# Optimization experiments

Hardware: AMD Instinct MI355X
Metric: run time of the kernel (lower is better)

The kernel has to match this reference:

```python
import jax, jax.numpy as jnp
import numpy as np

B = 4096      # batch
D = 64        # state_dim
H = 512       # hidden_dim


def setup_inputs() -> dict:
    key = jax.random.key(0)
    ks = jax.random.split(key, 16)

    def init(k, shape, fan_in):
        return jax.random.normal(k, shape, dtype=jnp.float32) / np.float32(np.sqrt(fan_in))

    mu = jax.random.normal(ks[0], (B, D), dtype=jnp.float32)
    sigma_diag = 0.1 * jax.random.uniform(ks[1], (B, D), dtype=jnp.float32) + 0.01
    states = jnp.concatenate([mu, sigma_diag], axis=1)  # [B, 2D]

    return {
        "t": jnp.float32(0.5),
        "states": states,
        # dynamics net: tanh MLP D -> H -> H -> D
        "W1": init(ks[2], (H, D), D), "b1": jnp.zeros((H,), jnp.float32),
        "W2": init(ks[3], (H, H), H), "b2": jnp.zeros((H,), jnp.float32),
        "W3": init(ks[4], (D, H), H), "b3": jnp.zeros((D,), jnp.float32),
        # process-noise net: tanh MLP D -> H -> H -> D, softplus head (diagonal Q)
        "V1": init(ks[5], (H, D), D), "c1": jnp.zeros((H,), jnp.float32),
        "V2": init(ks[6], (H, H), H), "c2": jnp.zeros((H,), jnp.float32),
        "V3": init(ks[7], (D, H), H), "c3": jnp.zeros((D,), jnp.float32),
    }


def reference(t, states, W1, b1, W2, b2, W3, b3, V1, c1, V2, c2, V3, c3):
    # UPN ODE function, diagonal-covariance path.
    mu = states[:, :D]          # [B, D]
    sigma_diag = states[:, D:]  # [B, D]

    # dynamics MLP forward (t is an autonomous-system placeholder, unused)
    h1 = jnp.tanh(mu @ W1.T + b1)   # [B, H]
    h2 = jnp.tanh(h1 @ W2.T + b2)   # [B, H]
    mu_drift = h2 @ W3.T + b3       # [B, D]

    # analytic batched Jacobian of the tanh MLP: J = W3 diag(1-h2^2) W2 diag(1-h1^2) W1
    d1 = 1.0 - h1 * h1              # [B, H]
    d2 = 1.0 - h2 * h2              # [B, H]
    inner = jnp.einsum('hk,bk,kd->bhd', W2, d1, W1)   # [B, H, D]
    J = jnp.einsum('oh,bh,bhd->bod', W3, d2, inner)   # [B, D, D]
    J_diag = jnp.diagonal(J, axis1=1, axis2=2)        # [B, D]

    # process-noise net: diagonal Q, softplus ensures positivity
    g1 = jnp.tanh(mu @ V1.T + c1)
    g2 = jnp.tanh(g1 @ V2.T + c2)
    Q_diag = jax.nn.softplus(g2 @ V3.T + c3)          # [B, D]

    sigma_drift = 2.0 * J_diag * sigma_diag + Q_diag  # [B, D]
    return jnp.concatenate([mu_drift, sigma_drift], axis=1)  # [B, 2D]
```

## Files before the change

### kernel.cpp

```cpp
#include <hip/hip_runtime.h>
#include <hip/hip_bf16.h>

#define BB 4096
#define DD 64
#define HH 512

typedef __hip_bfloat16 bf16;
typedef _Float16 f16;
typedef __attribute__((ext_vector_type(8))) short bf16x8;
typedef __attribute__((ext_vector_type(8))) _Float16 f16x8;
typedef __attribute__((ext_vector_type(4))) float f32x4;

__device__ __forceinline__ float bf2f(bf16 x) { return __bfloat162float(x); }
__device__ __forceinline__ float u16tof(unsigned short u) {
  union { unsigned int i; float f; } v; v.i = ((unsigned int)u) << 16; return v.f;
}
#define BC8(p) __builtin_bit_cast(bf16x8, *(const uint4*)(p))
#define BCH8(p) __builtin_bit_cast(f16x8, *(const uint4*)(p))

__device__ __forceinline__ void gl16(const void* g, void* l) {
  __builtin_amdgcn_global_load_lds((__attribute__((address_space(1))) void*)g,
                                   (__attribute__((address_space(3))) void*)l,
                                   16, 0, 0);
}


__global__ __launch_bounds__(256) void cvt_weights(
    const float* __restrict__ W2, const float* __restrict__ V2,
    const float* __restrict__ W1, const float* __restrict__ V1,
    const float* __restrict__ W3, const float* __restrict__ V3,
    bf16* __restrict__ W2bf, bf16* __restrict__ V2bf,
    bf16* __restrict__ W1bf, bf16* __restrict__ V1bf,
    bf16* __restrict__ W3bf, bf16* __restrict__ V3bf,
    f16* __restrict__ W2fr, f16* __restrict__ W1sw, float* __restrict__ W3T) {
  int blk = blockIdx.x, t = threadIdx.x;
  if (blk < 512) {
    const float* src = (blk < 256) ? W2 : V2;
    bf16* dst = (blk < 256) ? W2bf : V2bf;
    int i = ((blk & 255) * 256 + t) * 4;
    float4 v = *(const float4*)(src + i);
    bf16 o[4] = {__float2bfloat16(v.x), __float2bfloat16(v.y),
                 __float2bfloat16(v.z), __float2bfloat16(v.w)};
    *(uint2*)(dst + i) = *(uint2*)o;
  } else if (blk < 640) {
    int uid = (blk - 512) * 256 + t;
    int col = (uid >> 2) & 511;
    int kc2s = uid >> 11;
    int kc = kc2s >> 1, s = kc2s & 1, q = uid & 3;
    const float* src = W2 + (size_t)col * HH + kc * 64 + s * 32 + q * 8;
    float4 a = *(const float4*)src;
    float4 b = *(const float4*)(src + 4);
    f16 o[8] = {(f16)a.x, (f16)a.y, (f16)a.z, (f16)a.w,
                (f16)b.x, (f16)b.y, (f16)b.z, (f16)b.w};
    *(uint4*)(W2fr + (size_t)uid * 8) = *(uint4*)o;
  } else if (blk < 656) {
    int uid = (blk - 640) * 256 + t;
    int kc = uid >> 9, rem = uid & 511;
    int dl = rem >> 3, u = rem & 7;
    f16 o[8];
#pragma unroll
    for (int e = 0; e < 8; ++e)
      o[e] = (f16)W1[(size_t)(kc * 64 + u * 8 + e) * DD + dl];
    *(uint4*)(W1sw + (size_t)((kc * 64 + dl) * 8 + (u ^ (dl & 7))) * 8) = *(uint4*)o;
  } else if (blk < 784) {
    int which = (blk - 656) >> 5;
    int local = (blk - 656) & 31;
    const float* src = (which == 0) ? W1 : (which == 1) ? V1 : (which == 2) ? W3 : V3;
    bf16* dst = (which == 0) ? W1bf : (which == 1) ? V1bf : (which == 2) ? W3bf : V3bf;
    int i = (local * 256 + t) * 4;
    float4 v = *(const float4*)(src + i);
    bf16 o[4] = {__float2bfloat16(v.x), __float2bfloat16(v.y),
                 __float2bfloat16(v.z), __float2bfloat16(v.w)};
    *(uint2*)(dst + i) = *(uint2*)o;
  } else {
    int e = ((blk - 784) * 256 + t) * 4;
    int h = e >> 6, o0 = e & 63;
    float o[4];
#pragma unroll
    for (int j = 0; j < 4; ++j) o[j] = W3[(size_t)(o0 + j) * HH + h];
    *(float4*)(W3T + (size_t)h * 64 + o0) = *(float4*)o;
  }
}

__global__ __launch_bounds__(256) void fwd(
    const float* __restrict__ states,
    const bf16* __restrict__ W1bf, const float* __restrict__ b1,
    const bf16* __restrict__ W2bf, const float* __restrict__ b2,
    const bf16* __restrict__ W3bf, const float* __restrict__ b3,
    const bf16* __restrict__ V1bf, const float* __restrict__ c1,
    const bf16* __restrict__ V2bf, const float* __restrict__ c2,
    const bf16* __restrict__ V3bf, const float* __restrict__ c3,
    bf16* __restrict__ Xbf, bf16* __restrict__ Ybf, float* __restrict__ out) {
  __shared__ __align__(16) bf16 mus[16 * 72];
  __shared__ __align__(16) bf16 Xres[16 * 520];
  __shared__ __align__(16) bf16 Bs[128 * 72];
  __shared__ __align__(16) bf16 Ych[16 * 136];
  const int bt = blockIdx.x * 16;
  const int path = blockIdx.y;
  const bf16* Wa = path ? V1bf : W1bf;
  const float* ba = path ? c1 : b1;
  const bf16* Wb = path ? V2bf : W2bf;
  const float* bbv = path ? c2 : b2;
  const bf16* Wc = path ? V3bf : W3bf;
  const float* bcv = path ? c3 : b3;
  const int t = threadIdx.x;
  const int lane = t & 63;
  const int w = t >> 6;
  const int c = lane & 15, q = lane >> 4;

  if (t < 128) {
    int row = t >> 3, cg = (t & 7) * 8;
    bf16 o[8];
#pragma unroll
    for (int j = 0; j < 8; j += 4) {
      float4 v = *(const float4*)(states + (size_t)(bt + row) * 128 + cg + j);
      o[j] = __float2bfloat16(v.x); o[j + 1] = __float2bfloat16(v.y);
      o[j + 2] = __float2bfloat16(v.z); o[j + 3] = __float2bfloat16(v.w);
    }
    *(uint4*)(mus + row * 72 + cg) = *(const uint4*)o;
  }
  __syncthreads();

  for (int nch = 0; nch < 4; ++nch) {
    if (nch) __syncthreads();
#pragma unroll
    for (int i = 0; i < 4; ++i) {
      int g = t + i * 256;
      int row = g >> 3, kb = (g & 7) * 8;
      *(uint4*)(Bs + row * 72 + kb) =
          *(const uint4*)(Wa + (size_t)(nch * 128 + row) * 64 + kb);
    }
    __syncthreads();
    f32x4 acc1[2] = {};
#pragma unroll
    for (int s = 0; s < 2; ++s) {
      bf16x8 af = BC8(mus + c * 72 + s * 32 + q * 8);
#pragma unroll
      for (int nt = 0; nt < 2; ++nt) {
        bf16x8 bfr = BC8(Bs + (w * 32 + nt * 16 + c) * 72 + s * 32 + q * 8);
        acc1[nt] = __builtin_amdgcn_mfma_f32_16x16x32_bf16(af, bfr, acc1[nt], 0, 0, 0);
      }
    }
#pragma unroll
    for (int nt = 0; nt < 2; ++nt) {
      int col = nch * 128 + w * 32 + nt * 16 + c;
      float bias = ba[col];
#pragma unroll
      for (int r = 0; r < 4; ++r) {
        int row = q * 4 + r;
        float x = tanhf(acc1[nt][r] + bias);
        Xres[row * 520 + col] = __float2bfloat16(x);
        if (!path) Xbf[(size_t)(bt + row) * HH + col] = __float2bfloat16(x);
      }
    }
  }
  __syncthreads();

  f32x4 acc3 = {};
  for (int hch = 0; hch < 4; ++hch) {
    f32x4 acc2[2] = {};
    for (int kc = 0; kc < 8; ++kc) {
      __syncthreads();
#pragma unroll
      for (int i = 0; i < 4; ++i) {
        int g = t + i * 256;
        int row = g >> 3, kb = (g & 7) * 8;
        *(uint4*)(Bs + row * 72 + kb) =
            *(const uint4*)(Wb + (size_t)(hch * 128 + row) * HH + kc * 64 + kb);
      }
      __syncthreads();
#pragma unroll
      for (int s = 0; s < 2; ++s) {
        bf16x8 af = BC8(Xres + c * 520 + kc * 64 + s * 32 + q * 8);
#pragma unroll
        for (int nt = 0; nt < 2; ++nt) {
          bf16x8 bfr = BC8(Bs + (w * 32 + nt * 16 + c) * 72 + s * 32 + q * 8);
          acc2[nt] = __builtin_amdgcn_mfma_f32_16x16x32_bf16(af, bfr, acc2[nt], 0, 0, 0);
        }
      }
    }
    __syncthreads();
#pragma unroll
    for (int nt = 0; nt < 2; ++nt) {
      int hl = w * 32 + nt * 16 + c;
      int h = hch * 128 + hl;
      float bias = bbv[h];
#pragma unroll
      for (int r = 0; r < 4; ++r) {
        int row = q * 4 + r;
        float y = tanhf(acc2[nt][r] + bias);
        Ych[row * 136 + hl] = __float2bfloat16(y);
        if (!path) Ybf[(size_t)(bt + row) * HH + h] = __float2bfloat16(y);
      }
    }
    __syncthreads();
#pragma unroll
    for (int s3 = 0; s3 < 4; ++s3) {
      bf16x8 bf3 = BC8(Wc + (size_t)(w * 16 + c) * HH + hch * 128 + s3 * 32 + q * 8);
      bf16x8 af3 = BC8(Ych + c * 136 + s3 * 32 + q * 8);
      acc3 = __builtin_amdgcn_mfma_f32_16x16x32_bf16(af3, bf3, acc3, 0, 0, 0);
    }
  }
  {
    int o = w * 16 + c;
    float bias = bcv[o];
#pragma unroll
    for (int r = 0; r < 4; ++r) {
      int row = q * 4 + r;
      float v = acc3[r] + bias;
      if (path) {
        v = fmaxf(v, 0.0f) + log1pf(expf(-fabsf(v)));
        out[(size_t)(bt + row) * 128 + 64 + o] = v;
      } else {
        out[(size_t)(bt + row) * 128 + o] = v;
      }
    }
  }
}

#define LDSW1 0
#define LDSD1 65536
#define LDSD2 73728
#define LDSRED 77824

__global__ __launch_bounds__(512, 2) void k4_gemm(
    const bf16* __restrict__ Xbf, const bf16* __restrict__ Ybf,
    const f16* __restrict__ W1sw, const f16* __restrict__ W2fr,
    const float* __restrict__ W3T, float* __restrict__ Jpart) {
  __shared__ __align__(16) char lds[81920];
  const int bt = blockIdx.x;
  const int h0 = blockIdx.y * 256;
  const int t = threadIdx.x;
  const int lane = t & 63;
  const int w = t >> 6;
  const int c = lane & 15, q = lane >> 4;
  const int wr = w >> 2, wc = w & 3;
  const int b0 = bt * 4;

#pragma unroll
  for (int i = 0; i < 8; ++i)
    gl16((const char*)W1sw + (t + i * 512) * 16,
         (char*)lds + LDSW1 + (t + i * 512) * 16);
  {
    int e = t * 4, j = e >> 9, k = e & 511;
    ushort4 xv = *(const ushort4*)((const unsigned short*)Xbf +
                                   (size_t)(b0 + j) * HH + k);
    f16 o[4];
    float x;
    x = u16tof(xv.x); o[0] = (f16)(1.f - x * x);
    x = u16tof(xv.y); o[1] = (f16)(1.f - x * x);
    x = u16tof(xv.z); o[2] = (f16)(1.f - x * x);
    x = u16tof(xv.w); o[3] = (f16)(1.f - x * x);
    *(uint2*)(lds + LDSD1 + e * 2) = *(uint2*)o;
  }
  {
    int e = t * 2, j = e >> 8, n = e & 255;
    ushort2 yv = *(const ushort2*)((const unsigned short*)Ybf +
                                   (size_t)(b0 + j) * HH + h0 + n);
    float y0 = u16tof(yv.x), y1 = u16tof(yv.y);
    float2 d2v = {1.f - y0 * y0, 1.f - y1 * y1};
    *(float2*)(lds + LDSD2 + e * 4) = d2v;
  }
  __syncthreads();

  const int cj = c & 7;
  const int j16_0 = ((0 + q) ^ cj) * 16;
  const int j16_1 = ((4 + q) ^ cj) * 16;
  const int arow = c * 128;
  const char* d1b = (const char*)lds + LDSD1 + wr * 2048 + q * 16;

  const char* gB = (const char*)W2fr + (size_t)(h0 + wc * 64) * 64 +
                   (c * 64 + q * 16);
#define BLD(kc_, s_, nt_) \
  BCH8(gB + ((kc_) * 2 + (s_)) * 32768 + (nt_) * 1024)

  f16x8 bb0[2][4], bb1[2][4];
#pragma unroll
  for (int nt = 0; nt < 4; ++nt) bb0[0][nt] = BLD(0, 0, nt);
#pragma unroll
  for (int nt = 0; nt < 4; ++nt) bb1[0][nt] = BLD(0, 1, nt);

  f32x4 acc[8][4] = {};

#pragma unroll
  for (int kc = 0; kc < 8; ++kc) {
    const int cur = kc & 1, nxt = cur ^ 1;
    if (kc < 7) {
#pragma unroll
      for (int nt = 0; nt < 4; ++nt) bb0[nxt][nt] = BLD(kc + 1, 0, nt);
#pragma unroll
      for (int nt = 0; nt < 4; ++nt) bb1[nxt][nt] = BLD(kc + 1, 1, nt);
    }
    const char* Ab = (const char*)lds + LDSW1 + kc * 8192;
    f16x8 a0[4], a1[4];
#pragma unroll
    for (int i = 0; i < 4; ++i) a0[i] = BCH8(Ab + arow + i * 2048 + j16_0);
#pragma unroll
    for (int i = 0; i < 4; ++i) a1[i] = BCH8(Ab + arow + i * 2048 + j16_1);
    f16x8 d00 = BCH8(d1b + kc * 128);
    f16x8 d10 = BCH8(d1b + 1024 + kc * 128);
    f16x8 d01 = BCH8(d1b + 64 + kc * 128);
    f16x8 d11 = BCH8(d1b + 1024 + 64 + kc * 128);

    f16x8 av;
    __builtin_amdgcn_s_setprio(1);
#pragma unroll
    for (int mt = 0; mt < 4; ++mt) {
      av = a0[mt] * d00;
#pragma unroll
      for (int nt = 0; nt < 4; ++nt)
        acc[mt][nt] = __builtin_amdgcn_mfma_f32_16x16x32_f16(
            av, bb0[cur][nt], acc[mt][nt], 0, 0, 0);
    }
#pragma unroll
    for (int mt = 0; mt < 4; ++mt) {
      av = a0[mt] * d10;
#pragma unroll
      for (int nt = 0; nt < 4; ++nt)
        acc[mt + 4][nt] = __builtin_amdgcn_mfma_f32_16x16x32_f16(
            av, bb0[cur][nt], acc[mt + 4][nt], 0, 0, 0);
    }
#pragma unroll
    for (int mt = 0; mt < 4; ++mt) {
      av = a1[mt] * d01;
#pragma unroll
      for (int nt = 0; nt < 4; ++nt)
        acc[mt][nt] = __builtin_amdgcn_mfma_f32_16x16x32_f16(
            av, bb1[cur][nt], acc[mt][nt], 0, 0, 0);
    }
#pragma unroll
    for (int mt = 0; mt < 4; ++mt) {
      av = a1[mt] * d11;
#pragma unroll
      for (int nt = 0; nt < 4; ++nt)
        acc[mt + 4][nt] = __builtin_amdgcn_mfma_f32_16x16x32_f16(
            av, bb1[cur][nt], acc[mt + 4][nt], 0, 0, 0);
    }
    __builtin_amdgcn_s_setprio(0);
    __builtin_amdgcn_sched_barrier(0);
  }
  __syncthreads();

#pragma unroll
  for (int i = 0; i < 8; ++i) {
    int e = (t + i * 512) * 4;
    int col = e >> 6, dl0 = e & 63;
    float4 v = *(const float4*)(W3T + (size_t)(h0 + col) * 64 + dl0);
    *(float4*)(lds + (col * 72 + dl0) * 4) = v;
  }
  __syncthreads();

  float d2r[2][4];
#pragma unroll
  for (int bh = 0; bh < 2; ++bh)
#pragma unroll
    for (int nt = 0; nt < 4; ++nt)
      d2r[bh][nt] = *(const float*)(
          lds + LDSD2 + ((wr * 2 + bh) * 256 + wc * 64 + nt * 16 + c) * 4);

  float vsum[8][4] = {};
#pragma unroll
  for (int mt4 = 0; mt4 < 4; ++mt4)
#pragma unroll
    for (int nt = 0; nt < 4; ++nt) {
      f32x4 w3v = *(const f32x4*)(
          lds + ((wc * 64 + nt * 16 + c) * 72 + mt4 * 16 + q * 4) * 4);
#pragma unroll
      for (int bh = 0; bh < 2; ++bh) {
        const int mt = bh * 4 + mt4;
        float sc = d2r[bh][nt];
#pragma unroll
        for (int r = 0; r < 4; ++r)
          vsum[mt][r] += acc[mt][nt][r] * w3v[r] * sc;
      }
    }

#pragma unroll
  for (int mt = 0; mt < 8; ++mt)
#pragma unroll
    for (int r = 0; r < 4; ++r) {
      float v = vsum[mt][r];
      v += __shfl_xor(v, 1);
      v += __shfl_xor(v, 2);
      v += __shfl_xor(v, 4);
      v += __shfl_xor(v, 8);
      if (c == 0)
        *(float*)(lds + LDSRED +
                  (wc * 256 + wr * 128 + mt * 16 + q * 4 + r) * 4) = v;
    }
  __syncthreads();
  if (t < 256) {
    float J = *(const float*)(lds + LDSRED + t * 4) +
              *(const float*)(lds + LDSRED + (256 + t) * 4) +
              *(const float*)(lds + LDSRED + (512 + t) * 4) +
              *(const float*)(lds + LDSRED + (768 + t) * 4);
    Jpart[(size_t)blockIdx.y * (BB * 64) + (size_t)bt * 256 + t] = J;
  }
}

__global__ __launch_bounds__(256) void combine(
    const float* __restrict__ Jpart, const float* __restrict__ states,
    float* __restrict__ out) {
  int idx = blockIdx.x * 256 + threadIdx.x;
  int b = idx >> 6, d = idx & 63;
  const int plane = BB * 64;
  float J = Jpart[idx] + Jpart[plane + idx];
  float sig = states[(size_t)b * 128 + 64 + d];
  float qd = out[(size_t)b * 128 + 64 + d];
  out[(size_t)b * 128 + 64 + d] = 2.0f * J * sig + qd;
}

extern "C" void kernel_launch(void* const* d_in, const int* in_sizes, int n_in,
                              void* d_out, int out_size, void* d_ws, size_t ws_size,
                              hipStream_t stream) {
  const float* states = (const float*)d_in[1];
  const float* W1 = (const float*)d_in[2];
  const float* b1 = (const float*)d_in[3];
  const float* W2 = (const float*)d_in[4];
  const float* b2 = (const float*)d_in[5];
  const float* W3 = (const float*)d_in[6];
  const float* b3 = (const float*)d_in[7];
  const float* V1 = (const float*)d_in[8];
  const float* c1 = (const float*)d_in[9];
  const float* V2 = (const float*)d_in[10];
  const float* c2 = (const float*)d_in[11];
  const float* V3 = (const float*)d_in[12];
  const float* c3 = (const float*)d_in[13];
  float* out = (float*)d_out;

  bf16* Xbf = (bf16*)d_ws;
  bf16* Ybf = Xbf + (size_t)BB * HH;
  bf16* W2bf = Ybf + (size_t)BB * HH;
  bf16* V2bf = W2bf + (size_t)HH * HH;
  bf16* W1bf = V2bf + (size_t)HH * HH;
  bf16* V1bf = W1bf + (size_t)HH * DD;
  bf16* W3bf = V1bf + (size_t)HH * DD;
  bf16* V3bf = W3bf + (size_t)DD * HH;
  f16* W1sw = (f16*)(V3bf + (size_t)DD * HH);
  f16* W2fr = W1sw + (size_t)DD * HH;
  float* W3T = (float*)(W2fr + (size_t)HH * HH);
  float* Jpart = W3T + (size_t)HH * DD;

  cvt_weights<<<dim3(816), 256, 0, stream>>>(W2, V2, W1, V1, W3, V3,
                                             W2bf, V2bf, W1bf, V1bf,
                                             W3bf, V3bf, W2fr, W1sw, W3T);
  fwd<<<dim3(256, 2), 256, 0, stream>>>(states, W1bf, b1, W2bf, b2, W3bf, b3,
                                        V1bf, c1, V2bf, c2, V3bf, c3,
                                        Xbf, Ybf, out);
  k4_gemm<<<dim3(1024, 2), 512, 0, stream>>>(Xbf, Ybf, W1sw, W2fr, W3T, Jpart);
  combine<<<dim3(1024), 256, 0, stream>>>(Jpart, states, out);
}
```

Before: 269.2 us.

## Split Jacobian GEMM per batch row and K-half for more blocks

The Jacobian-diagonal kernel now gives each block a single batch row and half of the hidden K range, with 256 threads instead of 512. That makes a 4096x2x2 grid of smaller-LDS blocks meant to raise occupancy, and the combine kernel now sums four partial planes. W3 is read straight from global memory instead of being staged in LDS. In exchange, each W2 fragment and the staged W1 tile are reused across one batch row instead of four, which multiplies global/L2 traffic. The Jpart workspace also doubles.

After: 369.5 us. 37.2% more time.

```diff
diff --git a/kernel.cpp b/kernel.cpp
--- a/kernel.cpp
+++ b/kernel.cpp
@@ -219,47 +219,42 @@
 }
 
 #define LDSW1 0
-#define LDSD1 65536
-#define LDSD2 73728
-#define LDSRED 77824
-
-__global__ __launch_bounds__(512, 2) void k4_gemm(
+#define LDSD1 32768
+#define LDSD2 33280
+#define LDSRED 34304
+
+__global__ __launch_bounds__(256, 3) void k4_gemm(
     const bf16* __restrict__ Xbf, const bf16* __restrict__ Ybf,
     const f16* __restrict__ W1sw, const f16* __restrict__ W2fr,
     const float* __restrict__ W3T, float* __restrict__ Jpart) {
-  __shared__ __align__(16) char lds[81920];
-  const int bt = blockIdx.x;
+  __shared__ __align__(16) char lds[35328];
+  const int b = blockIdx.x;
   const int h0 = blockIdx.y * 256;
+  const int kh = blockIdx.z;
+  const int k0 = kh * 4;
   const int t = threadIdx.x;
   const int lane = t & 63;
-  const int w = t >> 6;
+  const int wc = t >> 6;
   const int c = lane & 15, q = lane >> 4;
-  const int wr = w >> 2, wc = w & 3;
-  const int b0 = bt * 4;
 
 #pragma unroll
   for (int i = 0; i < 8; ++i)
-    gl16((const char*)W1sw + (t + i * 512) * 16,
-         (char*)lds + LDSW1 + (t + i * 512) * 16);
-  {
-    int e = t * 4, j = e >> 9, k = e & 511;
+    gl16((const char*)W1sw + kh * 32768 + (t + i * 256) * 16,
+         (char*)lds + LDSW1 + (t + i * 256) * 16);
+  if (t < 64) {
     ushort4 xv = *(const ushort4*)((const unsigned short*)Xbf +
-                                   (size_t)(b0 + j) * HH + k);
+                                   (size_t)b * HH + kh * 256 + t * 4);
     f16 o[4];
     float x;
     x = u16tof(xv.x); o[0] = (f16)(1.f - x * x);
     x = u16tof(xv.y); o[1] = (f16)(1.f - x * x);
     x = u16tof(xv.z); o[2] = (f16)(1.f - x * x);
     x = u16tof(xv.w); o[3] = (f16)(1.f - x * x);
-    *(uint2*)(lds + LDSD1 + e * 2) = *(uint2*)o;
+    *(uint2*)(lds + LDSD1 + t * 8) = *(uint2*)o;
   }
   {
-    int e = t * 2, j = e >> 8, n = e & 255;
-    ushort2 yv = *(const ushort2*)((const unsigned short*)Ybf +
-                                   (size_t)(b0 + j) * HH + h0 + n);
-    float y0 = u16tof(yv.x), y1 = u16tof(yv.y);
-    float2 d2v = {1.f - y0 * y0, 1.f - y1 * y1};
-    *(float2*)(lds + LDSD2 + e * 4) = d2v;
+    float y = bf2f(Ybf[(size_t)b * HH + h0 + t]);
+    *(float*)(lds + LDSD2 + t * 4) = 1.f - y * y;
   }
   __syncthreads();
 
@@ -267,116 +262,82 @@
   const int j16_0 = ((0 + q) ^ cj) * 16;
   const int j16_1 = ((4 + q) ^ cj) * 16;
   const int arow = c * 128;
-  const char* d1b = (const char*)lds + LDSD1 + wr * 2048 + q * 16;
 
   const char* gB = (const char*)W2fr + (size_t)(h0 + wc * 64) * 64 +
                    (c * 64 + q * 16);
-#define BLD(kc_, s_, nt_) \
-  BCH8(gB + ((kc_) * 2 + (s_)) * 32768 + (nt_) * 1024)
-
-  f16x8 bb0[2][4], bb1[2][4];
-#pragma unroll
-  for (int nt = 0; nt < 4; ++nt) bb0[0][nt] = BLD(0, 0, nt);
-#pragma unroll
-  for (int nt = 0; nt < 4; ++nt) bb1[0][nt] = BLD(0, 1, nt);
-
-  f32x4 acc[8][4] = {};
-
-#pragma unroll
-  for (int kc = 0; kc < 8; ++kc) {
-    const int cur = kc & 1, nxt = cur ^ 1;
-    if (kc < 7) {
-#pragma unroll
-      for (int nt = 0; nt < 4; ++nt) bb0[nxt][nt] = BLD(kc + 1, 0, nt);
-#pragma unroll
-      for (int nt = 0; nt < 4; ++nt) bb1[nxt][nt] = BLD(kc + 1, 1, nt);
-    }
+#define BLD(kcg_, s_, nt_) \
+  BCH8(gB + ((kcg_) * 2 + (s_)) * 32768 + (nt_) * 1024)
+
+  f16x8 bA[4], bB[4];
+#pragma unroll
+  for (int nt = 0; nt < 4; ++nt) bA[nt] = BLD(k0, 0, nt);
+#pragma unroll
+  for (int nt = 0; nt < 4; ++nt) bB[nt] = BLD(k0, 1, nt);
+
+  f32x4 acc[4][4] = {};
+
+#pragma unroll
+  for (int kc = 0; kc < 4; ++kc) {
     const char* Ab = (const char*)lds + LDSW1 + kc * 8192;
     f16x8 a0[4], a1[4];
 #pragma unroll
     for (int i = 0; i < 4; ++i) a0[i] = BCH8(Ab + arow + i * 2048 + j16_0);
+    f16x8 d0 = BCH8(lds + LDSD1 + kc * 128 + q * 16);
 #pragma unroll
     for (int i = 0; i < 4; ++i) a1[i] = BCH8(Ab + arow + i * 2048 + j16_1);
-    f16x8 d00 = BCH8(d1b + kc * 128);
-    f16x8 d10 = BCH8(d1b + 1024 + kc * 128);
-    f16x8 d01 = BCH8(d1b + 64 + kc * 128);
-    f16x8 d11 = BCH8(d1b + 1024 + 64 + kc * 128);
-
-    f16x8 av;
+    f16x8 d1v = BCH8(lds + LDSD1 + kc * 128 + 64 + q * 16);
+
     __builtin_amdgcn_s_setprio(1);
 #pragma unroll
     for (int mt = 0; mt < 4; ++mt) {
-      av = a0[mt] * d00;
+      f16x8 av = a0[mt] * d0;
 #pragma unroll
       for (int nt = 0; nt < 4; ++nt)
         acc[mt][nt] = __builtin_amdgcn_mfma_f32_16x16x32_f16(
-            av, bb0[cur][nt], acc[mt][nt], 0, 0, 0);
-    }
+            av, bA[nt], acc[mt][nt], 0, 0, 0);
+    }
+    __builtin_amdgcn_s_setprio(0);
+    if (kc < 3) {
+#pragma unroll
+      for (int nt = 0; nt < 4; ++nt) bA[nt] = BLD(k0 + kc + 1, 0, nt);
+    }
+    __builtin_amdgcn_s_setprio(1);
 #pragma unroll
     for (int mt = 0; mt < 4; ++mt) {
-      av = a0[mt] * d10;
-#pragma unroll
-      for (int nt = 0; nt < 4; ++nt)
-        acc[mt + 4][nt] = __builtin_amdgcn_mfma_f32_16x16x32_f16(
-            av, bb0[cur][nt], acc[mt + 4][nt], 0, 0, 0);
-    }
-#pragma unroll
-    for (int mt = 0; mt < 4; ++mt) {
-      av = a1[mt] * d01;
+      f16x8 av = a1[mt] * d1v;
 #pragma unroll
       for (int nt = 0; nt < 4; ++nt)
         acc[mt][nt] = __builtin_amdgcn_mfma_f32_16x16x32_f16(
-            av, bb1[cur][nt], acc[mt][nt], 0, 0, 0);
-    }
-#pragma unroll
-    for (int mt = 0; mt < 4; ++mt) {
-      av = a1[mt] * d11;
-#pragma unroll
-      for (int nt = 0; nt < 4; ++nt)
-        acc[mt + 4][nt] = __builtin_amdgcn_mfma_f32_16x16x32_f16(
-            av, bb1[cur][nt], acc[mt + 4][nt], 0, 0, 0);
+            av, bB[nt], acc[mt][nt], 0, 0, 0);
     }
     __builtin_amdgcn_s_setprio(0);
+    if (kc < 3) {
+#pragma unroll
+      for (int nt = 0; nt < 4; ++nt) bB[nt] = BLD(k0 + kc + 1, 1, nt);
+    }
     __builtin_amdgcn_sched_barrier(0);
   }
-  __syncthreads();
-
-#pragma unroll
-  for (int i = 0; i < 8; ++i) {
-    int e = (t + i * 512) * 4;
-    int col = e >> 6, dl0 = e & 63;
-    float4 v = *(const float4*)(W3T + (size_t)(h0 + col) * 64 + dl0);
-    *(float4*)(lds + (col * 72 + dl0) * 4) = v;
-  }
-  __syncthreads();
-
-  float d2r[2][4];
-#pragma unroll
-  for (int bh = 0; bh < 2; ++bh)
-#pragma unroll
-    for (int nt = 0; nt < 4; ++nt)
-      d2r[bh][nt] = *(const float*)(
-          lds + LDSD2 + ((wr * 2 + bh) * 256 + wc * 64 + nt * 16 + c) * 4);
-
-  float vsum[8][4] = {};
-#pragma unroll
-  for (int mt4 = 0; mt4 < 4; ++mt4)
+
+  float d2r[4];
+#pragma unroll
+  for (int nt = 0; nt < 4; ++nt)
+    d2r[nt] = *(const float*)(lds + LDSD2 + (wc * 64 + nt * 16 + c) * 4);
+
+  float vsum[4][4] = {};
+#pragma unroll
+  for (int mt = 0; mt < 4; ++mt)
 #pragma unroll
     for (int nt = 0; nt < 4; ++nt) {
       f32x4 w3v = *(const f32x4*)(
-          lds + ((wc * 64 + nt * 16 + c) * 72 + mt4 * 16 + q * 4) * 4);
-#pragma unroll
-      for (int bh = 0; bh < 2; ++bh) {
-        const int mt = bh * 4 + mt4;
-        float sc = d2r[bh][nt];
-#pragma unroll
-        for (int r = 0; r < 4; ++r)
-          vsum[mt][r] += acc[mt][nt][r] * w3v[r] * sc;
-      }
-    }
-
-#pragma unroll
-  for (int mt = 0; mt < 8; ++mt)
+          W3T + (size_t)(h0 + wc * 64 + nt * 16 + c) * 64 + mt * 16 + q * 4);
+      float sc = d2r[nt];
+#pragma unroll
+      for (int r = 0; r < 4; ++r)
+        vsum[mt][r] += acc[mt][nt][r] * w3v[r] * sc;
+    }
+
+#pragma unroll
+  for (int mt = 0; mt < 4; ++mt)
 #pragma unroll
     for (int r = 0; r < 4; ++r) {
       float v = vsum[mt][r];
@@ -385,16 +346,15 @@
       v += __shfl_xor(v, 4);
       v += __shfl_xor(v, 8);
       if (c == 0)
-        *(float*)(lds + LDSRED +
-                  (wc * 256 + wr * 128 + mt * 16 + q * 4 + r) * 4) = v;
+        *(float*)(lds + LDSRED + (wc * 64 + mt * 16 + q * 4 + r) * 4) = v;
     }
   __syncthreads();
-  if (t < 256) {
+  if (t < 64) {
     float J = *(const float*)(lds + LDSRED + t * 4) +
-              *(const float*)(lds + LDSRED + (256 + t) * 4) +
-              *(const float*)(lds + LDSRED + (512 + t) * 4) +
-              *(const float*)(lds + LDSRED + (768 + t) * 4);
-    Jpart[(size_t)blockIdx.y * (BB * 64) + (size_t)bt * 256 + t] = J;
+              *(const float*)(lds + LDSRED + (64 + t) * 4) +
+              *(const float*)(lds + LDSRED + (128 + t) * 4) +
+              *(const float*)(lds + LDSRED + (192 + t) * 4);
+    Jpart[(size_t)(blockIdx.y * 2 + kh) * (BB * 64) + (size_t)b * 64 + t] = J;
   }
 }
 
@@ -404,7 +364,8 @@
   int idx = blockIdx.x * 256 + threadIdx.x;
   int b = idx >> 6, d = idx & 63;
   const int plane = BB * 64;
-  float J = Jpart[idx] + Jpart[plane + idx];
+  float J = Jpart[idx] + Jpart[plane + idx] + Jpart[2 * plane + idx] +
+            Jpart[3 * plane + idx];
   float sig = states[(size_t)b * 128 + 64 + d];
   float qd = out[(size_t)b * 128 + 64 + d];
   out[(size_t)b * 128 + 64 + d] = 2.0f * J * sig + qd;
@@ -447,6 +408,6 @@
   fwd<<<dim3(256, 2), 256, 0, stream>>>(states, W1bf, b1, W2bf, b2, W3bf, b3,
                                         V1bf, c1, V2bf, c2, V3bf, c3,
                                         Xbf, Ybf, out);
-  k4_gemm<<<dim3(1024, 2), 512, 0, stream>>>(Xbf, Ybf, W1sw, W2fr, W3T, Jpart);
+  k4_gemm<<<dim3(4096, 2, 2), 256, 0, stream>>>(Xbf, Ybf, W1sw, W2fr, W3T, Jpart);
   combine<<<dim3(1024), 256, 0, stream>>>(Jpart, states, out);
 }
```

## Restructure forward MLP kernel to read fragment-packed weights directly from global

Applied to the files above, without the earlier changes.

The weight-conversion kernel now emits W1/V1/W2/V2 in an MFMA-fragment-packed bf16 layout. This lets the forward kernel load B operands straight from global memory instead of staging them through LDS with repeated syncs. The forward kernel moves to 512 threads, so each wave owns 64 hidden columns. The third layer is split across waves along K and finished with an LDS reduction. The s_setprio hints in the Jacobian GEMM are also removed. The trade-off is more global/L2 traffic per block and a larger LDS footprint, in exchange for far fewer barriers.

Measured after the change: 263.1 us (median of 3 runs). 1.02x faster.

```diff
diff --git a/kernel.cpp b/kernel.cpp
--- a/kernel.cpp
+++ b/kernel.cpp
@@ -29,32 +29,23 @@
     const float* __restrict__ W2, const float* __restrict__ V2,
     const float* __restrict__ W1, const float* __restrict__ V1,
     const float* __restrict__ W3, const float* __restrict__ V3,
-    bf16* __restrict__ W2bf, bf16* __restrict__ V2bf,
-    bf16* __restrict__ W1bf, bf16* __restrict__ V1bf,
-    bf16* __restrict__ W3bf, bf16* __restrict__ V3bf,
-    f16* __restrict__ W2fr, f16* __restrict__ W1sw, float* __restrict__ W3T) {
+    f16* __restrict__ W2fr, f16* __restrict__ W1sw, float* __restrict__ W3T,
+    bf16* __restrict__ W2fb, bf16* __restrict__ V2fb,
+    bf16* __restrict__ W1fb, bf16* __restrict__ V1fb,
+    bf16* __restrict__ W3bf, bf16* __restrict__ V3bf) {
   int blk = blockIdx.x, t = threadIdx.x;
-  if (blk < 512) {
-    const float* src = (blk < 256) ? W2 : V2;
-    bf16* dst = (blk < 256) ? W2bf : V2bf;
-    int i = ((blk & 255) * 256 + t) * 4;
-    float4 v = *(const float4*)(src + i);
-    bf16 o[4] = {__float2bfloat16(v.x), __float2bfloat16(v.y),
-                 __float2bfloat16(v.z), __float2bfloat16(v.w)};
-    *(uint2*)(dst + i) = *(uint2*)o;
-  } else if (blk < 640) {
-    int uid = (blk - 512) * 256 + t;
+  if (blk < 128) {
+    int uid = blk * 256 + t;
     int col = (uid >> 2) & 511;
-    int kc2s = uid >> 11;
-    int kc = kc2s >> 1, s = kc2s & 1, q = uid & 3;
-    const float* src = W2 + (size_t)col * HH + kc * 64 + s * 32 + q * 8;
+    int ks = uid >> 11, q = uid & 3;
+    const float* src = W2 + (size_t)col * HH + ks * 32 + q * 8;
     float4 a = *(const float4*)src;
     float4 b = *(const float4*)(src + 4);
     f16 o[8] = {(f16)a.x, (f16)a.y, (f16)a.z, (f16)a.w,
                 (f16)b.x, (f16)b.y, (f16)b.z, (f16)b.w};
     *(uint4*)(W2fr + (size_t)uid * 8) = *(uint4*)o;
-  } else if (blk < 656) {
-    int uid = (blk - 640) * 256 + t;
+  } else if (blk < 144) {
+    int uid = (blk - 128) * 256 + t;
     int kc = uid >> 9, rem = uid & 511;
     int dl = rem >> 3, u = rem & 7;
     f16 o[8];
@@ -62,44 +53,74 @@
     for (int e = 0; e < 8; ++e)
       o[e] = (f16)W1[(size_t)(kc * 64 + u * 8 + e) * DD + dl];
     *(uint4*)(W1sw + (size_t)((kc * 64 + dl) * 8 + (u ^ (dl & 7))) * 8) = *(uint4*)o;
-  } else if (blk < 784) {
-    int which = (blk - 656) >> 5;
-    int local = (blk - 656) & 31;
-    const float* src = (which == 0) ? W1 : (which == 1) ? V1 : (which == 2) ? W3 : V3;
-    bf16* dst = (which == 0) ? W1bf : (which == 1) ? V1bf : (which == 2) ? W3bf : V3bf;
+  } else if (blk < 208) {
+    int which = (blk - 144) >> 5;
+    int local = (blk - 144) & 31;
+    const float* src = (which == 0) ? W3 : V3;
+    bf16* dst = (which == 0) ? W3bf : V3bf;
     int i = (local * 256 + t) * 4;
     float4 v = *(const float4*)(src + i);
     bf16 o[4] = {__float2bfloat16(v.x), __float2bfloat16(v.y),
                  __float2bfloat16(v.z), __float2bfloat16(v.w)};
     *(uint2*)(dst + i) = *(uint2*)o;
-  } else {
-    int e = ((blk - 784) * 256 + t) * 4;
+  } else if (blk < 240) {
+    int e = ((blk - 208) * 256 + t) * 4;
     int h = e >> 6, o0 = e & 63;
     float o[4];
 #pragma unroll
     for (int j = 0; j < 4; ++j) o[j] = W3[(size_t)(o0 + j) * HH + h];
     *(float4*)(W3T + (size_t)h * 64 + o0) = *(float4*)o;
-  }
-}
-
-__global__ __launch_bounds__(256) void fwd(
+  } else if (blk < 496) {
+    int uid = (blk - 240) * 256 + t;
+    const float* S = (uid < 32768) ? W2 : V2;
+    bf16* D = (uid < 32768) ? W2fb : V2fb;
+    uid &= 32767;
+    int col = (uid >> 2) & 511;
+    int ks = uid >> 11, q = uid & 3;
+    const float* src = S + (size_t)col * HH + ks * 32 + q * 8;
+    float4 a = *(const float4*)src;
+    float4 b = *(const float4*)(src + 4);
+    bf16 o[8] = {__float2bfloat16(a.x), __float2bfloat16(a.y),
+                 __float2bfloat16(a.z), __float2bfloat16(a.w),
+                 __float2bfloat16(b.x), __float2bfloat16(b.y),
+                 __float2bfloat16(b.z), __float2bfloat16(b.w)};
+    *(uint4*)(D + (size_t)uid * 8) = *(uint4*)o;
+  } else {
+    int uid = (blk - 496) * 256 + t;
+    const float* S = (uid < 4096) ? W1 : V1;
+    bf16* D = (uid < 4096) ? W1fb : V1fb;
+    uid &= 4095;
+    int col = (uid >> 2) & 511;
+    int ks = uid >> 11, q = uid & 3;
+    const float* src = S + (size_t)col * DD + ks * 32 + q * 8;
+    float4 a = *(const float4*)src;
+    float4 b = *(const float4*)(src + 4);
+    bf16 o[8] = {__float2bfloat16(a.x), __float2bfloat16(a.y),
+                 __float2bfloat16(a.z), __float2bfloat16(a.w),
+                 __float2bfloat16(b.x), __float2bfloat16(b.y),
+                 __float2bfloat16(b.z), __float2bfloat16(b.w)};
+    *(uint4*)(D + (size_t)uid * 8) = *(uint4*)o;
+  }
+}
+
+__global__ __launch_bounds__(512, 4) void fwd(
     const float* __restrict__ states,
-    const bf16* __restrict__ W1bf, const float* __restrict__ b1,
-    const bf16* __restrict__ W2bf, const float* __restrict__ b2,
+    const bf16* __restrict__ W1fb, const float* __restrict__ b1,
+    const bf16* __restrict__ W2fb, const float* __restrict__ b2,
     const bf16* __restrict__ W3bf, const float* __restrict__ b3,
-    const bf16* __restrict__ V1bf, const float* __restrict__ c1,
-    const bf16* __restrict__ V2bf, const float* __restrict__ c2,
+    const bf16* __restrict__ V1fb, const float* __restrict__ c1,
+    const bf16* __restrict__ V2fb, const float* __restrict__ c2,
     const bf16* __restrict__ V3bf, const float* __restrict__ c3,
     bf16* __restrict__ Xbf, bf16* __restrict__ Ybf, float* __restrict__ out) {
   __shared__ __align__(16) bf16 mus[16 * 72];
   __shared__ __align__(16) bf16 Xres[16 * 520];
-  __shared__ __align__(16) bf16 Bs[128 * 72];
-  __shared__ __align__(16) bf16 Ych[16 * 136];
+  __shared__ __align__(16) bf16 Ych[16 * 520];
+  __shared__ __align__(16) float red[8 * 16 * 66];
   const int bt = blockIdx.x * 16;
   const int path = blockIdx.y;
-  const bf16* Wa = path ? V1bf : W1bf;
+  const bf16* Wa = path ? V1fb : W1fb;
   const float* ba = path ? c1 : b1;
-  const bf16* Wb = path ? V2bf : W2bf;
+  const bf16* Wb = path ? V2fb : W2fb;
   const float* bbv = path ? c2 : b2;
   const bf16* Wc = path ? V3bf : W3bf;
   const float* bcv = path ? c3 : b3;
@@ -121,99 +142,85 @@
   }
   __syncthreads();
 
-  for (int nch = 0; nch < 4; ++nch) {
-    if (nch) __syncthreads();
-#pragma unroll
-    for (int i = 0; i < 4; ++i) {
-      int g = t + i * 256;
-      int row = g >> 3, kb = (g & 7) * 8;
-      *(uint4*)(Bs + row * 72 + kb) =
-          *(const uint4*)(Wa + (size_t)(nch * 128 + row) * 64 + kb);
-    }
-    __syncthreads();
-    f32x4 acc1[2] = {};
-#pragma unroll
-    for (int s = 0; s < 2; ++s) {
-      bf16x8 af = BC8(mus + c * 72 + s * 32 + q * 8);
-#pragma unroll
-      for (int nt = 0; nt < 2; ++nt) {
-        bf16x8 bfr = BC8(Bs + (w * 32 + nt * 16 + c) * 72 + s * 32 + q * 8);
-        acc1[nt] = __builtin_amdgcn_mfma_f32_16x16x32_bf16(af, bfr, acc1[nt], 0, 0, 0);
-      }
-    }
-#pragma unroll
-    for (int nt = 0; nt < 2; ++nt) {
-      int col = nch * 128 + w * 32 + nt * 16 + c;
-      float bias = ba[col];
-#pragma unroll
-      for (int r = 0; r < 4; ++r) {
-        int row = q * 4 + r;
-        float x = tanhf(acc1[nt][r] + bias);
-        Xres[row * 520 + col] = __float2bfloat16(x);
-        if (!path) Xbf[(size_t)(bt + row) * HH + col] = __float2bfloat16(x);
-      }
-    }
-  }
-  __syncthreads();
-
-  f32x4 acc3 = {};
-  for (int hch = 0; hch < 4; ++hch) {
-    f32x4 acc2[2] = {};
-    for (int kc = 0; kc < 8; ++kc) {
-      __syncthreads();
-#pragma unroll
-      for (int i = 0; i < 4; ++i) {
-        int g = t + i * 256;
-        int row = g >> 3, kb = (g & 7) * 8;
-        *(uint4*)(Bs + row * 72 + kb) =
-            *(const uint4*)(Wb + (size_t)(hch * 128 + row) * HH + kc * 64 + kb);
-      }
-      __syncthreads();
-#pragma unroll
-      for (int s = 0; s < 2; ++s) {
-        bf16x8 af = BC8(Xres + c * 520 + kc * 64 + s * 32 + q * 8);
-#pragma unroll
-        for (int nt = 0; nt < 2; ++nt) {
-          bf16x8 bfr = BC8(Bs + (w * 32 + nt * 16 + c) * 72 + s * 32 + q * 8);
-          acc2[nt] = __builtin_amdgcn_mfma_f32_16x16x32_bf16(af, bfr, acc2[nt], 0, 0, 0);
-        }
-      }
-    }
-    __syncthreads();
-#pragma unroll
-    for (int nt = 0; nt < 2; ++nt) {
-      int hl = w * 32 + nt * 16 + c;
-      int h = hch * 128 + hl;
-      float bias = bbv[h];
-#pragma unroll
-      for (int r = 0; r < 4; ++r) {
-        int row = q * 4 + r;
-        float y = tanhf(acc2[nt][r] + bias);
-        Ych[row * 136 + hl] = __float2bfloat16(y);
-        if (!path) Ybf[(size_t)(bt + row) * HH + h] = __float2bfloat16(y);
-      }
-    }
-    __syncthreads();
-#pragma unroll
-    for (int s3 = 0; s3 < 4; ++s3) {
-      bf16x8 bf3 = BC8(Wc + (size_t)(w * 16 + c) * HH + hch * 128 + s3 * 32 + q * 8);
-      bf16x8 af3 = BC8(Ych + c * 136 + s3 * 32 + q * 8);
-      acc3 = __builtin_amdgcn_mfma_f32_16x16x32_bf16(af3, bf3, acc3, 0, 0, 0);
-    }
-  }
-  {
-    int o = w * 16 + c;
-    float bias = bcv[o];
+  f32x4 acc1[4] = {};
+#pragma unroll
+  for (int s = 0; s < 2; ++s) {
+    bf16x8 af = BC8(mus + c * 72 + s * 32 + q * 8);
+#pragma unroll
+    for (int nt = 0; nt < 4; ++nt) {
+      bf16x8 bfr = BC8(Wa + ((size_t)(s * 512 + w * 64 + nt * 16 + c) * 4 + q) * 8);
+      acc1[nt] = __builtin_amdgcn_mfma_f32_16x16x32_bf16(af, bfr, acc1[nt], 0, 0, 0);
+    }
+  }
+#pragma unroll
+  for (int nt = 0; nt < 4; ++nt) {
+    int col = w * 64 + nt * 16 + c;
+    float bias = ba[col];
 #pragma unroll
     for (int r = 0; r < 4; ++r) {
       int row = q * 4 + r;
-      float v = acc3[r] + bias;
-      if (path) {
-        v = fmaxf(v, 0.0f) + log1pf(expf(-fabsf(v)));
-        out[(size_t)(bt + row) * 128 + 64 + o] = v;
-      } else {
-        out[(size_t)(bt + row) * 128 + o] = v;
+      float x = tanhf(acc1[nt][r] + bias);
+      Xres[row * 520 + col] = __float2bfloat16(x);
+      if (!path) Xbf[(size_t)(bt + row) * HH + col] = __float2bfloat16(x);
+    }
+  }
+  __syncthreads();
+
+  f32x4 acc2[4] = {};
+  for (int kc = 0; kc < 8; ++kc) {
+#pragma unroll
+    for (int s = 0; s < 2; ++s) {
+      int ks = kc * 2 + s;
+      bf16x8 af = BC8(Xres + c * 520 + kc * 64 + s * 32 + q * 8);
+#pragma unroll
+      for (int nt = 0; nt < 4; ++nt) {
+        bf16x8 bfr = BC8(Wb + ((size_t)(ks * 512 + w * 64 + nt * 16 + c) * 4 + q) * 8);
+        acc2[nt] = __builtin_amdgcn_mfma_f32_16x16x32_bf16(af, bfr, acc2[nt], 0, 0, 0);
       }
+    }
+  }
+#pragma unroll
+  for (int nt = 0; nt < 4; ++nt) {
+    int col = w * 64 + nt * 16 + c;
+    float bias = bbv[col];
+#pragma unroll
+    for (int r = 0; r < 4; ++r) {
+      int row = q * 4 + r;
+      float y = tanhf(acc2[nt][r] + bias);
+      Ych[row * 520 + col] = __float2bfloat16(y);
+      if (!path) Ybf[(size_t)(bt + row) * HH + col] = __float2bfloat16(y);
+    }
+  }
+  __syncthreads();
+
+  f32x4 acc3[4] = {};
+#pragma unroll
+  for (int s3 = 0; s3 < 2; ++s3) {
+    bf16x8 af3 = BC8(Ych + c * 520 + w * 64 + s3 * 32 + q * 8);
+#pragma unroll
+    for (int nt = 0; nt < 4; ++nt) {
+      bf16x8 bf3 = BC8(Wc + (size_t)(nt * 16 + c) * HH + w * 64 + s3 * 32 + q * 8);
+      acc3[nt] = __builtin_amdgcn_mfma_f32_16x16x32_bf16(af3, bf3, acc3[nt], 0, 0, 0);
+    }
+  }
+#pragma unroll
+  for (int nt = 0; nt < 4; ++nt)
+#pragma unroll
+    for (int r = 0; r < 4; ++r)
+      red[w * 1056 + (q * 4 + r) * 66 + nt * 16 + c] = acc3[nt][r];
+  __syncthreads();
+
+#pragma unroll
+  for (int oidx = t; oidx < 1024; oidx += 512) {
+    int row = oidx >> 6, o = oidx & 63;
+    float v = bcv[o];
+#pragma unroll
+    for (int wp = 0; wp < 8; ++wp) v += red[wp * 1056 + row * 66 + o];
+    if (path) {
+      v = fmaxf(v, 0.0f) + log1pf(expf(-fabsf(v)));
+      out[(size_t)(bt + row) * 128 + 64 + o] = v;
+    } else {
+      out[(size_t)(bt + row) * 128 + o] = v;
     }
   }
 }
@@ -303,7 +310,6 @@
     f16x8 d11 = BCH8(d1b + 1024 + 64 + kc * 128);
 
     f16x8 av;
-    __builtin_amdgcn_s_setprio(1);
 #pragma unroll
     for (int mt = 0; mt < 4; ++mt) {
       av = a0[mt] * d00;
@@ -336,7 +342,6 @@
         acc[mt + 4][nt] = __builtin_amdgcn_mfma_f32_16x16x32_f16(
             av, bb1[cur][nt], acc[mt + 4][nt], 0, 0, 0);
     }
-    __builtin_amdgcn_s_setprio(0);
     __builtin_amdgcn_sched_barrier(0);
   }
   __syncthreads();
@@ -430,22 +435,23 @@
 
   bf16* Xbf = (bf16*)d_ws;
   bf16* Ybf = Xbf + (size_t)BB * HH;
-  bf16* W2bf = Ybf + (size_t)BB * HH;
-  bf16* V2bf = W2bf + (size_t)HH * HH;
-  bf16* W1bf = V2bf + (size_t)HH * HH;
-  bf16* V1bf = W1bf + (size_t)HH * DD;
-  bf16* W3bf = V1bf + (size_t)HH * DD;
-  bf16* V3bf = W3bf + (size_t)DD * HH;
-  f16* W1sw = (f16*)(V3bf + (size_t)DD * HH);
+  f16* W1sw = (f16*)(Ybf + (size_t)BB * HH);
   f16* W2fr = W1sw + (size_t)DD * HH;
   float* W3T = (float*)(W2fr + (size_t)HH * HH);
-  float* Jpart = W3T + (size_t)HH * DD;
-
-  cvt_weights<<<dim3(816), 256, 0, stream>>>(W2, V2, W1, V1, W3, V3,
-                                             W2bf, V2bf, W1bf, V1bf,
-                                             W3bf, V3bf, W2fr, W1sw, W3T);
-  fwd<<<dim3(256, 2), 256, 0, stream>>>(states, W1bf, b1, W2bf, b2, W3bf, b3,
-                                        V1bf, c1, V2bf, c2, V3bf, c3,
+  bf16* W2fb = (bf16*)(W3T + (size_t)HH * DD);
+  bf16* V2fb = W2fb + (size_t)HH * HH;
+  bf16* W1fb = V2fb + (size_t)HH * HH;
+  bf16* V1fb = W1fb + (size_t)HH * DD;
+  bf16* W3bf = V1fb + (size_t)HH * DD;
+  bf16* V3bf = W3bf + (size_t)DD * HH;
+  float* Jpart = (float*)(V3bf + (size_t)DD * HH);
+
+  cvt_weights<<<dim3(528), 256, 0, stream>>>(W2, V2, W1, V1, W3, V3,
+                                             W2fr, W1sw, W3T,
+                                             W2fb, V2fb, W1fb, V1fb,
+                                             W3bf, V3bf);
+  fwd<<<dim3(256, 2), 512, 0, stream>>>(states, W1fb, b1, W2fb, b2, W3bf, b3,
+                                        V1fb, c1, V2fb, c2, V3bf, c3,
                                         Xbf, Ybf, out);
   k4_gemm<<<dim3(1024, 2), 512, 0, stream>>>(Xbf, Ybf, W1sw, W2fr, W3T, Jpart);
   combine<<<dim3(1024), 256, 0, stream>>>(Jpart, states, out);
```
